# Kernel optimization log

Hardware: AMD Instinct MI355X
Metric: run time of the kernel (lower is better)

The kernel has to match this reference:

```python
import jax, jax.numpy as jnp
import numpy as np

N = 50000       # total nodes
D = 20000       # disease nodes (first D rows)
M = 30000       # mirna nodes
E = 800000      # edges
DSIM = 512; MSIM = 512
HID = 128; OUT = 128; P = 3   # powers p = [0,1,2]
PAIRS = 100000


def _lin(k, o, i):
    s = 1.0 / np.sqrt(i)
    return jax.random.uniform(k, (o, i), jnp.float32, -s, s)


def setup_inputs() -> dict:
    key = jax.random.key(0)
    ks = jax.random.split(key, 24)
    inp = {}
    inp["d_sim"] = jax.random.normal(ks[0], (N, DSIM), jnp.float32)
    inp["m_sim"] = jax.random.normal(ks[1], (N, MSIM), jnp.float32)
    inp["edge_src"] = jax.random.randint(ks[2], (E,), 0, N, jnp.int32)
    inp["edge_dst"] = jax.random.randint(ks[3], (E,), 0, N, jnp.int32)
    inp["src"] = jax.random.randint(ks[4], (PAIRS,), 0, D, jnp.int32)
    inp["dst"] = D + jax.random.randint(ks[5], (PAIRS,), 0, M, jnp.int32)
    # input projections
    inp["d_fc_w"] = _lin(ks[6], HID, DSIM); inp["d_fc_b"] = jnp.zeros((HID,), jnp.float32)
    inp["m_fc_w"] = _lin(ks[7], HID, MSIM); inp["m_fc_b"] = jnp.zeros((HID,), jnp.float32)
    # MixHopConv per-power weights (no bias)
    inp["l0_w"] = jnp.stack([_lin(ks[8 + j], OUT, HID) for j in range(P)])         # [P, OUT, HID]
    inp["l1_w"] = jnp.stack([_lin(ks[11 + j], HID, OUT * P) for j in range(P)])    # [P, HID, OUT*P]
    inp["fc_w"] = _lin(ks[14], OUT, HID * P)
    inp["d_fc1_w"] = _lin(ks[15], OUT, OUT + DSIM); inp["d_fc1_b"] = jnp.zeros((OUT,), jnp.float32)
    inp["m_fc1_w"] = _lin(ks[16], OUT, OUT + MSIM); inp["m_fc1_b"] = jnp.zeros((OUT,), jnp.float32)
    # predictor MLP
    inp["p0_w"] = _lin(ks[17], OUT, 2 * OUT); inp["p0_b"] = jnp.zeros((OUT,), jnp.float32)
    inp["p1_w"] = _lin(ks[18], 1, OUT); inp["p1_b"] = jnp.zeros((1,), jnp.float32)
    return inp


def _mixhop(feats, Ws, edge_src, edge_dst, norm):
    """DGL MixHopConv with p=[0,1,2]: outputs [W_j (D^-1/2 A D^-1/2)^j X for j in p], concatenated."""
    outs = []
    for j in range(P):
        outs.append(feats @ Ws[j].T)
        if j < P - 1:  # propagate one more hop (last hop's propagation is unused)
            feats = feats * norm
            feats = jax.ops.segment_sum(feats[edge_src], edge_dst, num_segments=N)
            feats = feats * norm
    return jnp.concatenate(outs, axis=1)


def reference(d_sim, m_sim, edge_src, edge_dst, src, dst,
              d_fc_w, d_fc_b, m_fc_w, m_fc_b, l0_w, l1_w, fc_w,
              d_fc1_w, d_fc1_b, m_fc1_w, m_fc1_b, p0_w, p0_b, p1_w, p1_b):
    # symmetric normalization from in-degrees (clamped to >= 1)
    degs = jax.ops.segment_sum(jnp.ones((E,), jnp.float32), edge_dst, num_segments=N)
    norm = (jnp.maximum(degs, 1.0) ** -0.5)[:, None]  # [N, 1]
    # per-node-type input projection (dropout = identity in eval)
    z_d = d_sim[:D] @ d_fc_w.T + d_fc_b
    z_m = m_sim[D:] @ m_fc_w.T + m_fc_b
    feats = jnp.concatenate([z_d, z_m], axis=0)               # [N, HID]
    feats = _mixhop(feats, l0_w, edge_src, edge_dst, norm)    # [N, OUT*P]
    feats = _mixhop(feats, l1_w, edge_src, edge_dst, norm)    # [N, HID*P]
    feats = feats @ fc_w.T                                    # [N, OUT]
    h_d = jax.nn.elu(jnp.concatenate([feats[:D], d_sim[:D]], axis=1) @ d_fc1_w.T + d_fc1_b)
    h_m = jax.nn.elu(jnp.concatenate([feats[D:], m_sim[D:]], axis=1) @ m_fc1_w.T + m_fc1_b)
    h = jnp.concatenate([h_d, h_m], axis=0)                   # [N, OUT]
    hc = jnp.concatenate([h[src], h[dst]], axis=1)            # [PAIRS, 2*OUT]
    score = jax.nn.sigmoid(jax.nn.relu(hc @ p0_w.T + p0_b) @ p1_w.T + p1_b)
    return score
```

## Files before the change

### kernel.cpp

```cpp
#include <hip/hip_runtime.h>
#include <cstddef>
#include <cstdint>

#define N_NODES 50000
#define D_NODES 20000
#define M_NODES 30000
#define E_EDGES 800000
#define PAIRS_N 100000

typedef unsigned short u16;
typedef unsigned int u32;
typedef short bf16x8 __attribute__((ext_vector_type(8)));
typedef float f32x4 __attribute__((ext_vector_type(4)));

__device__ __forceinline__ float bf2f(u16 u) {
  u32 v = ((u32)u) << 16;
  return __builtin_bit_cast(float, v);
}
__device__ __forceinline__ u16 f2bf(float f) {
  u32 u = __builtin_bit_cast(u32, f);
  u32 r = (u + 0x7fffu + ((u >> 16) & 1u)) >> 16;
  return (u16)r;
}
__device__ __forceinline__ u32 pk2(float x, float y) {
  return (u32)f2bf(x) | ((u32)f2bf(y) << 16);
}

__global__ void wprep_kernel(const float* dfc, const float* mfc,
                             const float* dfc1, const float* mfc1, const float* p0w,
                             u16* wdfc, u16* wmfc, u16* wdfc1s, u16* wmfc1s,
                             u16* wdfc1f, u16* wmfc1f, u16* wp0) {
  int i = blockIdx.x * 256 + threadIdx.x;
  const float* s; u16* d;
  if (i < 16384) {
    s = dfc + (size_t)i * 4; d = wdfc + (size_t)i * 4;
  } else if (i < 32768) {
    int l = i - 16384;
    s = mfc + (size_t)l * 4; d = wmfc + (size_t)l * 4;
  } else if (i < 49152) {
    int l = i - 32768, o = l >> 7, kq = l & 127;
    s = dfc1 + (size_t)o * 640 + 128 + kq * 4;
    d = wdfc1s + (size_t)o * 512 + kq * 4;
  } else if (i < 65536) {
    int l = i - 49152, o = l >> 7, kq = l & 127;
    s = mfc1 + (size_t)o * 640 + 128 + kq * 4;
    d = wmfc1s + (size_t)o * 512 + kq * 4;
  } else if (i < 69632) {
    int l = i - 65536, o = l >> 5, kq = l & 31;
    s = dfc1 + (size_t)o * 640 + kq * 4;
    d = wdfc1f + (size_t)o * 128 + kq * 4;
  } else if (i < 73728) {
    int l = i - 69632, o = l >> 5, kq = l & 31;
    s = mfc1 + (size_t)o * 640 + kq * 4;
    d = wmfc1f + (size_t)o * 128 + kq * 4;
  } else if (i < 81920) {
    int l = i - 73728;
    s = p0w + (size_t)l * 4; d = wp0 + (size_t)l * 4;
  } else return;
  float4 v = *(const float4*)s;
  ushort4 o4;
  o4.x = f2bf(v.x); o4.y = f2bf(v.y); o4.z = f2bf(v.z); o4.w = f2bf(v.w);
  *(ushort4*)d = o4;
}

__global__ void wcomb1_kernel(const float* __restrict__ l1w, const float* __restrict__ l0w,
                              float* __restrict__ Tmp) {
  int pj = blockIdx.x;
  int p = pj / 3, j = pj % 3;
  int o = blockIdx.y;
  int i = threadIdx.x;
  const float* wp = l1w + (size_t)p * 49152 + (size_t)o * 384 + 128 * j;
  const float* wj = l0w + (size_t)j * 16384 + i;
  float acc = 0.f;
#pragma unroll 4
  for (int t = 0; t < 128; ++t) acc += wp[t] * wj[(size_t)t * 128];
  Tmp[(size_t)pj * 16384 + (size_t)o * 128 + i] = acc;
}
__global__ void wcomb2_kernel(const float* __restrict__ fcw, const float* __restrict__ Tmp,
                              u16* __restrict__ G) {
  int k = blockIdx.x;
  int of = blockIdx.y;
  int i = threadIdx.x;
  float acc = 0.f;
  int plo = (k > 2) ? (k - 2) : 0;
  int phi = (k < 2) ? k : 2;
  for (int p = plo; p <= phi; ++p) {
    int j = k - p;
    const float* fp = fcw + (size_t)of * 384 + 128 * p;
    const float* tp = Tmp + (size_t)(p * 3 + j) * 16384 + i;
#pragma unroll 4
    for (int t = 0; t < 128; ++t) acc += fp[t] * tp[(size_t)t * 128];
  }
  G[(size_t)of * 640 + 128 * k + i] = f2bf(acc);
}

__global__ void zero_int_kernel(int* p, int n) {
  int i = blockIdx.x * 256 + threadIdx.x;
  if (i < n) p[i] = 0;
}
__global__ void deg_count_kernel(const int* __restrict__ dst, int* __restrict__ degs, int e) {
  int i = blockIdx.x * 256 + threadIdx.x;
  if (i < e) atomicAdd(&degs[dst[i]], 1);
}
__global__ void norm_reduce_kernel(const int* __restrict__ degs, float* __restrict__ norm,
                                   int n, int* __restrict__ bsums) {
  __shared__ int s[256];
  int t = threadIdx.x;
  int i = blockIdx.x * 256 + t;
  int d = (i < n) ? degs[i] : 0;
  if (i < n) norm[i] = rsqrtf(fmaxf((float)d, 1.0f));
  s[t] = d;
  __syncthreads();
  for (int st = 128; st > 0; st >>= 1) {
    if (t < st) s[t] += s[t + st];
    __syncthreads();
  }
  if (t == 0) bsums[blockIdx.x] = s[0];
}
__global__ void scan_small_kernel(int* b, int nb) {
  __shared__ int s[256];
  int t = threadIdx.x;
  int orig = (t < nb) ? b[t] : 0;
  s[t] = orig;
  __syncthreads();
  for (int st = 1; st < 256; st <<= 1) {
    int v = (t >= st) ? s[t - st] : 0;
    __syncthreads();
    s[t] += v;
    __syncthreads();
  }
  if (t < nb) b[t] = s[t] - orig;
}
__global__ void scan_final_kernel(const int* __restrict__ degs, const int* __restrict__ boff,
                                  int* __restrict__ out, int* __restrict__ cursor,
                                  int n, int total) {
  __shared__ int s[256];
  int t = threadIdx.x;
  int i = blockIdx.x * 256 + t;
  int orig = (i < n) ? degs[i] : 0;
  s[t] = orig;
  __syncthreads();
  for (int st = 1; st < 256; st <<= 1) {
    int v = (t >= st) ? s[t - st] : 0;
    __syncthreads();
    s[t] += v;
    __syncthreads();
  }
  if (i < n) {
    int v = boff[blockIdx.x] + s[t] - orig;
    out[i] = v;
    cursor[i] = v;
  }
  if (i == 0) out[n] = total;
}
__global__ void fill_csr_kernel(const int* __restrict__ esrc, const int* __restrict__ edst,
                                int* __restrict__ cursor, int* __restrict__ csr_src, int e) {
  int i = blockIdx.x * 256 + threadIdx.x;
  if (i < e) {
    int p = atomicAdd(&cursor[edst[i]], 1);
    csr_src[p] = esrc[i];
  }
}

__global__ void prop_kernel(const u16* __restrict__ in,
                            u16* __restrict__ outu, int ldu, int cOff,
                            u16* __restrict__ outs,
                            const int* __restrict__ off, const int* __restrict__ srcs,
                            const float* __restrict__ norm, int nnodes) {
  const int node = blockIdx.x * 4 + (threadIdx.x >> 6);
  if (node >= nnodes) return;
  const int lane = threadIdx.x & 63;
  const int e0 = off[node], e1 = off[node + 1];
  float a0 = 0.f, a1 = 0.f;
  const u16* basec = in + (lane << 1);
  for (int base = e0; base < e1; base += 64) {
    int nE = e1 - base; if (nE > 64) nE = 64;
    int myE = srcs[base + ((lane < nE) ? lane : (nE - 1))];
    int i = 0;
    for (; i + 8 <= nE; i += 8) {
      int s0 = __builtin_amdgcn_readlane(myE, i + 0);
      int s1 = __builtin_amdgcn_readlane(myE, i + 1);
      int s2 = __builtin_amdgcn_readlane(myE, i + 2);
      int s3 = __builtin_amdgcn_readlane(myE, i + 3);
      int s4 = __builtin_amdgcn_readlane(myE, i + 4);
      int s5 = __builtin_amdgcn_readlane(myE, i + 5);
      int s6 = __builtin_amdgcn_readlane(myE, i + 6);
      int s7 = __builtin_amdgcn_readlane(myE, i + 7);
      u32 v0 = *(const u32*)(basec + ((size_t)s0 << 7));
      u32 v1 = *(const u32*)(basec + ((size_t)s1 << 7));
      u32 v2 = *(const u32*)(basec + ((size_t)s2 << 7));
      u32 v3 = *(const u32*)(basec + ((size_t)s3 << 7));
      u32 v4 = *(const u32*)(basec + ((size_t)s4 << 7));
      u32 v5 = *(const u32*)(basec + ((size_t)s5 << 7));
      u32 v6 = *(const u32*)(basec + ((size_t)s6 << 7));
      u32 v7 = *(const u32*)(basec + ((size_t)s7 << 7));
      a0 += bf2f((u16)v0); a1 += bf2f((u16)(v0 >> 16));
      a0 += bf2f((u16)v1); a1 += bf2f((u16)(v1 >> 16));
      a0 += bf2f((u16)v2); a1 += bf2f((u16)(v2 >> 16));
      a0 += bf2f((u16)v3); a1 += bf2f((u16)(v3 >> 16));
      a0 += bf2f((u16)v4); a1 += bf2f((u16)(v4 >> 16));
      a0 += bf2f((u16)v5); a1 += bf2f((u16)(v5 >> 16));
      a0 += bf2f((u16)v6); a1 += bf2f((u16)(v6 >> 16));
      a0 += bf2f((u16)v7); a1 += bf2f((u16)(v7 >> 16));
    }
    for (; i < nE; ++i) {
      int s = __builtin_amdgcn_readlane(myE, i);
      u32 v = *(const u32*)(basec + ((size_t)s << 7));
      a0 += bf2f((u16)v); a1 += bf2f((u16)(v >> 16));
    }
  }
  float nd = norm[node];
  *(u32*)(outu + (size_t)node * ldu + cOff + (lane << 1)) = pk2(a0 * nd, a1 * nd);
  if (outs) {
    float nd2 = nd * nd;
    *(u32*)(outs + ((size_t)node << 7) + (lane << 1)) = pk2(a0 * nd2, a1 * nd2);
  }
}

__global__ __launch_bounds__(256) void proj_kernel(
    const float* __restrict__ dsim, const float* __restrict__ msim,
    const u16* __restrict__ Wdfc, const u16* __restrict__ Wmfc,
    const u16* __restrict__ Wdfc1s, const u16* __restrict__ Wmfc1s,
    const float* __restrict__ dfcb, const float* __restrict__ mfcb,
    int gdseg, int gseg,
    u16* __restrict__ HCAT, u16* __restrict__ HSa, float* __restrict__ SB,
    const float* __restrict__ normp) {
  __shared__ u32 As[32 * 32];
  __shared__ u32 Ws[128 * 32];
  const int tid = threadIdx.x;
  int b = (int)blockIdx.x;
  const bool sbseg = b >= gseg;
  if (sbseg) b -= gseg;
  const bool mseg = b >= gdseg;
  const int brow = mseg ? D_NODES + (b - gdseg) * 32 : b * 32;
  const int bound = mseg ? N_NODES : D_NODES;
  const float* A = mseg ? msim : dsim;
  const u16* W = sbseg ? (mseg ? Wmfc1s : Wdfc1s) : (mseg ? Wmfc : Wdfc);
  const float* bias = mseg ? mfcb : dfcb;

  const int lane = tid & 63, wv = tid >> 6;
  const int fr = lane & 15, fg = lane >> 4;
  const int sr = tid >> 3, sk = tid & 7;
  const int swc = tid >> 1, sh = tid & 1;
  const int prow = (brow + sr < bound) ? (brow + sr) : (bound - 1);

  const float* ap = A + (size_t)prow * 512 + sk * 8;
  uint4 aq[8];
#pragma unroll
  for (int j = 0; j < 8; ++j) {
    float4 f0 = ((const float4*)(ap + j * 64))[0];
    float4 f1 = ((const float4*)(ap + j * 64))[1];
    aq[j] = make_uint4(pk2(f0.x, f0.y), pk2(f0.z, f0.w), pk2(f1.x, f1.y), pk2(f1.z, f1.w));
  }

  const u16* wrow = W + (size_t)swc * 512 + sh * 32;
  uint4 pw0 = *(const uint4*)(wrow);
  uint4 pw1 = *(const uint4*)(wrow + 8);
  uint4 pw2 = *(const uint4*)(wrow + 16);
  uint4 pw3 = *(const uint4*)(wrow + 24);

  f32x4 acc[2][2];
#pragma unroll
  for (int m = 0; m < 2; ++m)
#pragma unroll
    for (int n = 0; n < 2; ++n) acc[m][n] = (f32x4){0.f, 0.f, 0.f, 0.f};

#pragma unroll
  for (int j = 0; j < 8; ++j) {
    __syncthreads();
    *(uint4*)&As[sr * 32 + (sk ^ (sr & 7)) * 4] = aq[j];
    *(uint4*)&Ws[swc * 32 + ((sh * 4 + 0) ^ (swc & 7)) * 4] = pw0;
    *(uint4*)&Ws[swc * 32 + ((sh * 4 + 1) ^ (swc & 7)) * 4] = pw1;
    *(uint4*)&Ws[swc * 32 + ((sh * 4 + 2) ^ (swc & 7)) * 4] = pw2;
    *(uint4*)&Ws[swc * 32 + ((sh * 4 + 3) ^ (swc & 7)) * 4] = pw3;
    __syncthreads();
    if (j < 7) {
      const u16* wp = wrow + (j + 1) * 64;
      pw0 = *(const uint4*)(wp);
      pw1 = *(const uint4*)(wp + 8);
      pw2 = *(const uint4*)(wp + 16);
      pw3 = *(const uint4*)(wp + 24);
    }
#pragma unroll
    for (int kk2 = 0; kk2 < 2; ++kk2) {
      int gix = kk2 * 4 + fg;
      int r0 = fr, r1 = 16 + fr;
      bf16x8 aF0 = *(const bf16x8*)&As[r0 * 32 + (gix ^ (r0 & 7)) * 4];
      bf16x8 aF1 = *(const bf16x8*)&As[r1 * 32 + (gix ^ (r1 & 7)) * 4];
#pragma unroll
      for (int n = 0; n < 2; ++n) {
        int cr = wv * 32 + n * 16 + fr;
        bf16x8 bF = *(const bf16x8*)&Ws[cr * 32 + (gix ^ (cr & 7)) * 4];
        acc[0][n] = __builtin_amdgcn_mfma_f32_16x16x32_bf16(aF0, bF, acc[0][n], 0, 0, 0);
        acc[1][n] = __builtin_amdgcn_mfma_f32_16x16x32_bf16(aF1, bF, acc[1][n], 0, 0, 0);
      }
    }
  }

#pragma unroll
  for (int m = 0; m < 2; ++m) {
#pragma unroll
    for (int n = 0; n < 2; ++n) {
      int ccol = wv * 32 + n * 16 + fr;
#pragma unroll
      for (int i = 0; i < 4; ++i) {
        int row = brow + m * 16 + fg * 4 + i;
        if (row < bound) {
          if (sbseg) {
            SB[((size_t)row << 7) + ccol] = acc[m][n][i];
          } else {
            float v = acc[m][n][i] + bias[ccol];
            HCAT[(size_t)row * 640 + ccol] = f2bf(v);
            HSa[((size_t)row << 7) + ccol] = f2bf(v * normp[row]);
          }
        }
      }
    }
  }
}

__global__ __launch_bounds__(256) void gemm128_kernel(
    const u16* __restrict__ A1, int lda1, int K1,
    const u16* __restrict__ A2, int lda2, int K2,
    const int* __restrict__ gsrc, const int* __restrict__ gdst,
    const u16* __restrict__ Wa, const u16* __restrict__ Wb,
    const float* __restrict__ biasa, const float* __restrict__ biasb,
    int splitB, int rowD, int boundA, int nrows,
    u16* __restrict__ Cu, int ldcu,
    const float* __restrict__ SBadd,
    const float* __restrict__ p1w, const float* __restrict__ p1b, float* __restrict__ outf,
    int act) {
  __shared__ u32 As[32 * 32];
  __shared__ u32 Ws[128 * 32];
  const int tid = threadIdx.x;
  const bool segb = (int)blockIdx.x >= splitB;
  const int brow = segb ? rowD + ((int)blockIdx.x - splitB) * 32 : (int)blockIdx.x * 32;
  const int bound = segb ? nrows : boundA;
  const u16* W = segb ? Wb : Wa;
  const float* bias = segb ? biasb : biasa;
  const int K = K1 + K2;
  const int lane = tid & 63;
  const int wv = tid >> 6;
  const int fr = lane & 15;
  const int fg = lane >> 4;

  f32x4 acc[2][2];
#pragma unroll
  for (int m = 0; m < 2; ++m)
#pragma unroll
    for (int n = 0; n < 2; ++n) acc[m][n] = (f32x4){0.f, 0.f, 0.f, 0.f};

  const int sr = tid >> 3, sk = tid & 7;
  const int swc = tid >> 1, sh = tid & 1;
  const int prow = (brow + sr < bound) ? (brow + sr) : (bound - 1);
  const int rA = gsrc ? gsrc[prow] : prow;
  const int rB = gsrc ? gdst[prow] : prow;

  for (int kc = 0; kc < K; kc += 64) {
    uint4 qa;
    {
      bool seg1 = kc < K1;
      int kk = (seg1 ? kc : kc - K1) + sk * 8;
      const u16* Av = seg1 ? A1 : A2;
      int ld = seg1 ? lda1 : lda2;
      int row = seg1 ? rA : rB;
      qa = *(const uint4*)(Av + (size_t)row * ld + kk);
    }
    const u16* wp = W + (size_t)swc * K + kc + sh * 32;
    uint4 qw0 = *(const uint4*)(wp);
    uint4 qw1 = *(const uint4*)(wp + 8);
    uint4 qw2 = *(const uint4*)(wp + 16);
    uint4 qw3 = *(const uint4*)(wp + 24);

    __syncthreads();
    *(uint4*)&As[sr * 32 + (sk ^ (sr & 7)) * 4] = qa;
    *(uint4*)&Ws[swc * 32 + ((sh * 4 + 0) ^ (swc & 7)) * 4] = qw0;
    *(uint4*)&Ws[swc * 32 + ((sh * 4 + 1) ^ (swc & 7)) * 4] = qw1;
    *(uint4*)&Ws[swc * 32 + ((sh * 4 + 2) ^ (swc & 7)) * 4] = qw2;
    *(uint4*)&Ws[swc * 32 + ((sh * 4 + 3) ^ (swc & 7)) * 4] = qw3;
    __syncthreads();

#pragma unroll
    for (int kk2 = 0; kk2 < 2; ++kk2) {
      int gix = kk2 * 4 + fg;
      int r0 = fr, r1 = 16 + fr;
      bf16x8 aF0 = *(const bf16x8*)&As[r0 * 32 + (gix ^ (r0 & 7)) * 4];
      bf16x8 aF1 = *(const bf16x8*)&As[r1 * 32 + (gix ^ (r1 & 7)) * 4];
#pragma unroll
      for (int n = 0; n < 2; ++n) {
        int cr = wv * 32 + n * 16 + fr;
        bf16x8 bF = *(const bf16x8*)&Ws[cr * 32 + (gix ^ (cr & 7)) * 4];
        acc[0][n] = __builtin_amdgcn_mfma_f32_16x16x32_bf16(aF0, bF, acc[0][n], 0, 0, 0);
        acc[1][n] = __builtin_amdgcn_mfma_f32_16x16x32_bf16(aF1, bF, acc[1][n], 0, 0, 0);
      }
    }
  }

  if (act == 3) {
    float part[2][4];
#pragma unroll
    for (int m = 0; m < 2; ++m)
#pragma unroll
      for (int i = 0; i < 4; ++i) part[m][i] = 0.f;
#pragma unroll
    for (int n = 0; n < 2; ++n) {
      int ccol = wv * 32 + n * 16 + fr;
      float b = bias[ccol];
      float pw = p1w[ccol];
#pragma unroll
      for (int m = 0; m < 2; ++m)
#pragma unroll
        for (int i = 0; i < 4; ++i) {
          float v = fmaxf(acc[m][n][i] + b, 0.f);
          part[m][i] += v * pw;
        }
    }
#pragma unroll
    for (int mask = 1; mask <= 8; mask <<= 1)
#pragma unroll
      for (int m = 0; m < 2; ++m)
#pragma unroll
        for (int i = 0; i < 4; ++i) part[m][i] += __shfl_xor(part[m][i], mask);
    __syncthreads();
    float* sred = (float*)As;
    if (fr == 0) {
#pragma unroll
      for (int m = 0; m < 2; ++m)
#pragma unroll
        for (int i = 0; i < 4; ++i) sred[wv * 32 + m * 16 + fg * 4 + i] = part[m][i];
    }
    __syncthreads();
    if (tid < 32) {
      int row = brow + tid;
      if (row < bound) {
        float s = sred[tid] + sred[32 + tid] + sred[64 + tid] + sred[96 + tid] + p1b[0];
        outf[row] = 1.f / (1.f + expf(-s));
      }
    }
    return;
  }

#pragma unroll
  for (int m = 0; m < 2; ++m) {
#pragma unroll
    for (int n = 0; n < 2; ++n) {
      int ccol = wv * 32 + n * 16 + fr;
      float b = bias ? bias[ccol] : 0.f;
#pragma unroll
      for (int i = 0; i < 4; ++i) {
        int row = brow + m * 16 + fg * 4 + i;
        if (row < bound) {
          float v = acc[m][n][i] + b;
          if (SBadd) v += SBadd[((size_t)row << 7) + ccol];
          if (act == 1) v = (v > 0.f) ? v : (expf(v) - 1.f);
          Cu[(size_t)row * ldcu + ccol] = f2bf(v);
        }
      }
    }
  }
}

extern "C" void kernel_launch(void* const* d_in, const int* in_sizes, int n_in,
                              void* d_out, int out_size, void* d_ws, size_t ws_size,
                              hipStream_t stream) {
  const float* d_sim   = (const float*)d_in[0];
  const float* m_sim   = (const float*)d_in[1];
  const int*   e_src   = (const int*)d_in[2];
  const int*   e_dst   = (const int*)d_in[3];
  const int*   p_src   = (const int*)d_in[4];
  const int*   p_dst   = (const int*)d_in[5];
  const float* d_fc_w  = (const float*)d_in[6];
  const float* d_fc_b  = (const float*)d_in[7];
  const float* m_fc_w  = (const float*)d_in[8];
  const float* m_fc_b  = (const float*)d_in[9];
  const float* l0_w    = (const float*)d_in[10];
  const float* l1_w    = (const float*)d_in[11];
  const float* fc_w    = (const float*)d_in[12];
  const float* d_fc1_w = (const float*)d_in[13];
  const float* d_fc1_b = (const float*)d_in[14];
  const float* m_fc1_w = (const float*)d_in[15];
  const float* m_fc1_b = (const float*)d_in[16];
  const float* p0_w    = (const float*)d_in[17];
  const float* p0_b    = (const float*)d_in[18];
  const float* p1_w    = (const float*)d_in[19];
  const float* p1_b    = (const float*)d_in[20];
  float* out = (float*)d_out;

  const int N = N_NODES, D = D_NODES, M = M_NODES, E = E_EDGES, NP = PAIRS_N;

  u16* ws16 = (u16*)d_ws;
  u16* HCAT = ws16;
  u16* HSa  = HCAT + (size_t)N * 640;
  u16* HSb  = HSa + (size_t)N * 128;
  u16* FE   = HSb + (size_t)N * 128;
  u16* HB   = FE  + (size_t)N * 128;
  u16* wb_dfc   = HB + (size_t)N * 128;
  u16* wb_mfc   = wb_dfc   + 65536;
  u16* wb_dfc1s = wb_mfc   + 65536;
  u16* wb_mfc1s = wb_dfc1s + 65536;
  u16* wb_dfc1f = wb_mfc1s + 65536;
  u16* wb_mfc1f = wb_dfc1f + 16384;
  u16* wb_p0    = wb_mfc1f + 16384;
  u16* wb_G     = wb_p0    + 32768;
  u16* wend     = wb_G     + 81920;
  size_t off16 = (size_t)(wend - ws16);
  off16 = (off16 + 1) & ~(size_t)1;
  float* SB    = (float*)(ws16 + off16);
  float* Tmp   = SB + (size_t)N * 128;
  float* normp = Tmp + 9 * 16384;
  int* degs    = (int*)(normp + N);
  int* csr_off = degs + N;
  int* cursor  = csr_off + N + 1;
  int* csr_src = cursor + N;
  int* bsums   = csr_src + E;

  const int nb = (N + 255) / 256;
  const int eb = (E + 255) / 256;

  wprep_kernel<<<320, 256, 0, stream>>>(d_fc_w, m_fc_w, d_fc1_w, m_fc1_w, p0_w,
                                        wb_dfc, wb_mfc, wb_dfc1s, wb_mfc1s,
                                        wb_dfc1f, wb_mfc1f, wb_p0);
  wcomb1_kernel<<<dim3(9, 128), 128, 0, stream>>>(l1_w, l0_w, Tmp);
  wcomb2_kernel<<<dim3(5, 128), 128, 0, stream>>>(fc_w, Tmp, wb_G);

  zero_int_kernel<<<nb, 256, 0, stream>>>(degs, N);
  deg_count_kernel<<<eb, 256, 0, stream>>>(e_dst, degs, E);
  norm_reduce_kernel<<<nb, 256, 0, stream>>>(degs, normp, N, bsums);
  scan_small_kernel<<<1, 256, 0, stream>>>(bsums, nb);
  scan_final_kernel<<<nb, 256, 0, stream>>>(degs, bsums, csr_off, cursor, N, E);
  fill_csr_kernel<<<eb, 256, 0, stream>>>(e_src, e_dst, cursor, csr_src, E);

  const int GDseg = D / 32;
  const int GMseg = (M + 31) / 32;
  const int GSEG = GDseg + GMseg;
  const int GN = (N + 31) / 32;
  const int GP = (NP + 31) / 32;
  const int GPROP = (N + 3) / 4;

  proj_kernel<<<2 * GSEG, 256, 0, stream>>>(
      d_sim, m_sim, wb_dfc, wb_mfc, wb_dfc1s, wb_mfc1s, d_fc_b, m_fc_b,
      GDseg, GSEG, HCAT, HSa, SB, normp);

  prop_kernel<<<GPROP, 256, 0, stream>>>(HSa, HCAT, 640, 128, HSb, csr_off, csr_src, normp, N);
  prop_kernel<<<GPROP, 256, 0, stream>>>(HSb, HCAT, 640, 256, HSa, csr_off, csr_src, normp, N);
  prop_kernel<<<GPROP, 256, 0, stream>>>(HSa, HCAT, 640, 384, HSb, csr_off, csr_src, normp, N);
  prop_kernel<<<GPROP, 256, 0, stream>>>(HSb, HCAT, 640, 512, nullptr, csr_off, csr_src, normp, N);

  gemm128_kernel<<<GN, 256, 0, stream>>>(
      HCAT, 640, 640, HCAT, 640, 0, nullptr, nullptr,
      wb_G, wb_G, nullptr, nullptr, GN, 0, N, N,
      FE, 128, nullptr, nullptr, nullptr, nullptr, 0);

  gemm128_kernel<<<GSEG, 256, 0, stream>>>(
      FE, 128, 128, FE, 128, 0, nullptr, nullptr,
      wb_dfc1f, wb_mfc1f, d_fc1_b, m_fc1_b, GDseg, D, D, N,
      HB, 128, SB, nullptr, nullptr, nullptr, 1);

  gemm128_kernel<<<GP, 256, 0, stream>>>(
      HB, 128, 128, HB, 128, 128, p_src, p_dst,
      wb_p0, wb_p0, p0_b, p0_b, GP, 0, NP, NP,
      nullptr, 128, nullptr, p1_w, p1_b, out, 3);

  (void)in_sizes; (void)n_in; (void)out_size; (void)ws_size;
}
```

Measured before the change: 395.9 us.

## Split graph propagation into column chunks with 16 lanes per node

The propagation kernel now gives each node 16 lanes covering a 32-column slice, with four column-chunk passes ordered chunk-major across the grid. Edge source indices are shared via shuffles, and 16 gathers are issued before any accumulation, replacing the 8-wide readlane batches. The aim is more loads in flight per wave, less work lost on low-degree nodes, and a smaller per-pass gather working set that stays cache resident. The grid size hardcodes the node count (3125*16 = N) and the bounds check is removed, so the kernel only works for this exact problem size.

```diff
diff --git a/kernel.cpp b/kernel.cpp
--- a/kernel.cpp
+++ b/kernel.cpp
@@ -166,54 +166,36 @@
                             u16* __restrict__ outu, int ldu, int cOff,
                             u16* __restrict__ outs,
                             const int* __restrict__ off, const int* __restrict__ srcs,
-                            const float* __restrict__ norm, int nnodes) {
-  const int node = blockIdx.x * 4 + (threadIdx.x >> 6);
-  if (node >= nnodes) return;
-  const int lane = threadIdx.x & 63;
+                            const float* __restrict__ norm) {
+  const int tid = threadIdx.x;
+  const int li = tid & 15;
+  const int blk = (int)blockIdx.x;
+  const int chunk = blk / 3125;
+  const int node = (blk % 3125) * 16 + (tid >> 4);
+  const int c0 = chunk * 32;
+  const int srcLaneBase = ((tid >> 4) & 3) << 4;
   const int e0 = off[node], e1 = off[node + 1];
   float a0 = 0.f, a1 = 0.f;
-  const u16* basec = in + (lane << 1);
-  for (int base = e0; base < e1; base += 64) {
-    int nE = e1 - base; if (nE > 64) nE = 64;
-    int myE = srcs[base + ((lane < nE) ? lane : (nE - 1))];
-    int i = 0;
-    for (; i + 8 <= nE; i += 8) {
-      int s0 = __builtin_amdgcn_readlane(myE, i + 0);
-      int s1 = __builtin_amdgcn_readlane(myE, i + 1);
-      int s2 = __builtin_amdgcn_readlane(myE, i + 2);
-      int s3 = __builtin_amdgcn_readlane(myE, i + 3);
-      int s4 = __builtin_amdgcn_readlane(myE, i + 4);
-      int s5 = __builtin_amdgcn_readlane(myE, i + 5);
-      int s6 = __builtin_amdgcn_readlane(myE, i + 6);
-      int s7 = __builtin_amdgcn_readlane(myE, i + 7);
-      u32 v0 = *(const u32*)(basec + ((size_t)s0 << 7));
-      u32 v1 = *(const u32*)(basec + ((size_t)s1 << 7));
-      u32 v2 = *(const u32*)(basec + ((size_t)s2 << 7));
-      u32 v3 = *(const u32*)(basec + ((size_t)s3 << 7));
-      u32 v4 = *(const u32*)(basec + ((size_t)s4 << 7));
-      u32 v5 = *(const u32*)(basec + ((size_t)s5 << 7));
-      u32 v6 = *(const u32*)(basec + ((size_t)s6 << 7));
-      u32 v7 = *(const u32*)(basec + ((size_t)s7 << 7));
-      a0 += bf2f((u16)v0); a1 += bf2f((u16)(v0 >> 16));
-      a0 += bf2f((u16)v1); a1 += bf2f((u16)(v1 >> 16));
-      a0 += bf2f((u16)v2); a1 += bf2f((u16)(v2 >> 16));
-      a0 += bf2f((u16)v3); a1 += bf2f((u16)(v3 >> 16));
-      a0 += bf2f((u16)v4); a1 += bf2f((u16)(v4 >> 16));
-      a0 += bf2f((u16)v5); a1 += bf2f((u16)(v5 >> 16));
-      a0 += bf2f((u16)v6); a1 += bf2f((u16)(v6 >> 16));
-      a0 += bf2f((u16)v7); a1 += bf2f((u16)(v7 >> 16));
-    }
-    for (; i < nE; ++i) {
-      int s = __builtin_amdgcn_readlane(myE, i);
-      u32 v = *(const u32*)(basec + ((size_t)s << 7));
-      a0 += bf2f((u16)v); a1 += bf2f((u16)(v >> 16));
+  const u16* basec = in + c0 + (li << 1);
+  for (int eb = e0; eb < e1; eb += 16) {
+    int nE = e1 - eb; if (nE > 16) nE = 16;
+    int myE = srcs[eb + ((li < nE) ? li : (nE - 1))];
+    u32 v[16];
+#pragma unroll
+    for (int i = 0; i < 16; ++i) {
+      int s = __shfl(myE, srcLaneBase + i, 64);
+      v[i] = *(const u32*)(basec + ((size_t)s << 7));
+    }
+#pragma unroll
+    for (int i = 0; i < 16; ++i) {
+      if (i < nE) { a0 += bf2f((u16)v[i]); a1 += bf2f((u16)(v[i] >> 16)); }
     }
   }
   float nd = norm[node];
-  *(u32*)(outu + (size_t)node * ldu + cOff + (lane << 1)) = pk2(a0 * nd, a1 * nd);
+  *(u32*)(outu + (size_t)node * ldu + cOff + c0 + (li << 1)) = pk2(a0 * nd, a1 * nd);
   if (outs) {
     float nd2 = nd * nd;
-    *(u32*)(outs + ((size_t)node << 7) + (lane << 1)) = pk2(a0 * nd2, a1 * nd2);
+    *(u32*)(outs + ((size_t)node << 7) + c0 + (li << 1)) = pk2(a0 * nd2, a1 * nd2);
   }
 }
 
@@ -535,16 +517,16 @@
   const int GSEG = GDseg + GMseg;
   const int GN = (N + 31) / 32;
   const int GP = (NP + 31) / 32;
-  const int GPROP = (N + 3) / 4;
+  const int GPROP = 4 * 3125;
 
   proj_kernel<<<2 * GSEG, 256, 0, stream>>>(
       d_sim, m_sim, wb_dfc, wb_mfc, wb_dfc1s, wb_mfc1s, d_fc_b, m_fc_b,
       GDseg, GSEG, HCAT, HSa, SB, normp);
 
-  prop_kernel<<<GPROP, 256, 0, stream>>>(HSa, HCAT, 640, 128, HSb, csr_off, csr_src, normp, N);
-  prop_kernel<<<GPROP, 256, 0, stream>>>(HSb, HCAT, 640, 256, HSa, csr_off, csr_src, normp, N);
-  prop_kernel<<<GPROP, 256, 0, stream>>>(HSa, HCAT, 640, 384, HSb, csr_off, csr_src, normp, N);
-  prop_kernel<<<GPROP, 256, 0, stream>>>(HSb, HCAT, 640, 512, nullptr, csr_off, csr_src, normp, N);
+  prop_kernel<<<GPROP, 256, 0, stream>>>(HSa, HCAT, 640, 128, HSb, csr_off, csr_src, normp);
+  prop_kernel<<<GPROP, 256, 0, stream>>>(HSb, HCAT, 640, 256, HSa, csr_off, csr_src, normp);
+  prop_kernel<<<GPROP, 256, 0, stream>>>(HSa, HCAT, 640, 384, HSb, csr_off, csr_src, normp);
+  prop_kernel<<<GPROP, 256, 0, stream>>>(HSb, HCAT, 640, 512, nullptr, csr_off, csr_src, normp);
 
   gemm128_kernel<<<GN, 256, 0, stream>>>(
       HCAT, 640, 640, HCAT, 640, 0, nullptr, nullptr,
```

After: 423.3 us. +6.9%, slower.
